# Performance work log

Measured on AMD Instinct MI355X. Metric: run time of the kernel, lower is better.

Reference implementation:

```python
import jax, jax.numpy as jnp
import numpy as np

M_HYP = 20  # RANSAC hypotheses
K_PTS = 4   # points per hypothesis


def _pdsac(pc, apc, idx):
    # pc, apc: [B, 3, N]; idx: [M_HYP*K_PTS] int point indices
    b, _, n = pc.shape
    dt = pc.dtype
    cog = jnp.sum(pc, axis=-1)            # [B,3]  (sum, not mean — faithful)
    c_pc = pc - cog[..., None]
    acog = jnp.sum(apc, axis=-1)
    c_apc = apc - acog[..., None]
    # gather then row-major reshape [B,3,80] -> [B,20,3,4] (mixes channel dim, faithful to torch .view)
    m_pc = c_pc[:, :, idx].reshape(b, M_HYP, 3, K_PTS)
    m_apc = c_apc[:, :, idx].reshape(b, M_HYP, 3, K_PTS)
    cov = jnp.einsum('bmck,bmdk->bmcd', m_pc, m_apc)          # [B,m,3,3]
    u, s, vh = jnp.linalg.svd(cov)
    rot = jnp.matmul(jnp.swapaxes(vh, -1, -2), jnp.swapaxes(u, -1, -2))  # V @ U^T
    rot = jnp.pad(rot, ((0, 0), (0, 0), (0, 1), (0, 0)))      # [B,m,4,3], zero bottom row
    trans = acog - cog                                         # [B,3]
    trans = jnp.broadcast_to(trans[:, None, :], (b, M_HYP, 3))
    trans = jnp.concatenate([trans, jnp.ones((b, M_HYP, 1), dt)], axis=-1)[..., None]  # [B,m,4,1]
    transform = jnp.concatenate([rot, trans], axis=-1)        # [B,m,4,4]
    pc_h = jnp.concatenate([pc, jnp.ones((b, 1, n), dt)], axis=1)   # [B,4,N]
    apc_h = jnp.concatenate([apc, jnp.ones((b, 1, n), dt)], axis=1)
    diff = jnp.einsum('bmcd,bdk->bmck', transform, pc_h) - apc_h[:, None]  # [B,m,4,N]
    errors = jnp.sqrt(jnp.sum(diff * diff, axis=(-2, -1)))    # Frobenius norm, [B,m]
    imin = jnp.argmin(errors, axis=-1)                        # [B]
    best = jnp.take_along_axis(transform, imin[:, None, None, None], axis=1)[:, 0]
    return best                                                # [B,4,4]


def setup_inputs() -> dict:
    key = jax.random.key(0)
    ks = jax.random.split(key, 6)
    bsz, n = 32, 100000
    A = jax.random.normal(ks[0], (bsz, 3, n), dtype=jnp.float32)
    A_g = jax.random.normal(ks[1], (bsz, 3, n), dtype=jnp.float32)
    B = jax.random.normal(ks[2], (bsz, 3, n), dtype=jnp.float32)
    B_g = jax.random.normal(ks[3], (bsz, 3, n), dtype=jnp.float32)
    idx_A = jax.random.randint(ks[4], (M_HYP * K_PTS,), 0, n, dtype=jnp.int32)
    idx_B = jax.random.randint(ks[5], (M_HYP * K_PTS,), 0, n, dtype=jnp.int32)
    return {"A": A, "A_g": A_g, "B": B, "B_g": B_g, "idx_A": idx_A, "idx_B": idx_B}


def reference(A, A_g, B, B_g, idx_A, idx_B):
    T_A = _pdsac(A, A_g, idx_A)
    T_B = _pdsac(B, B_g, idx_B)
    return jnp.matmul(jnp.linalg.inv(T_A), T_B)  # [B,4,4]
```

## Files before the change

### kernel.cpp

```cpp
#include <hip/hip_runtime.h>

#define M_HYP 20
#define AS1 __attribute__((address_space(1)))
#define AS3 __attribute__((address_space(3)))


__device__ __forceinline__ float comb8(const float r[8]) {
    return __fadd_rn(__fadd_rn(__fadd_rn(r[0], r[1]), __fadd_rn(r[2], r[3])),
                     __fadd_rn(__fadd_rn(r[4], r[5]), __fadd_rn(r[6], r[7])));
}

struct RawF { const float* a; };

__device__ __forceinline__ void raw8(const RawF& f, int k, float e[8]) {
    float4 v0 = *(const float4*)(f.a + k);
    float4 v1 = *(const float4*)(f.a + k + 4);
    e[0] = v0.x; e[1] = v0.y; e[2] = v0.z; e[3] = v0.w;
    e[4] = v1.x; e[5] = v1.y; e[6] = v1.z; e[7] = v1.w;
}

__device__ float leaf_raw(const RawF& f, int off, int n) {
    float r[8], e[8];
    raw8(f, off, e);
#pragma unroll
    for (int j = 0; j < 8; ++j) r[j] = e[j];
    for (int i = 8; i < n; i += 8) {
        raw8(f, off + i, e);
#pragma unroll
        for (int j = 0; j < 8; ++j) r[j] = __fadd_rn(r[j], e[j]);
    }
    return comb8(r);
}

__device__ float tree_raw(const RawF& f, int off0, int n0) {
    float lsum[14]; int roff[14], rn[14]; unsigned have = 0;
    int sp = 0, off = off0, n = n0;
    while (true) {
        while (n > 128) {
            int n2 = (n / 2) & ~7;
            roff[sp] = off + n2; rn[sp] = n - n2;
            have &= ~(1u << sp); ++sp;
            n = n2;
        }
        float s = leaf_raw(f, off, n);
        while (sp > 0 && (have & (1u << (sp - 1)))) {
            --sp; s = __fadd_rn(lsum[sp], s);
        }
        if (sp == 0) return s;
        lsum[sp - 1] = s; have |= (1u << (sp - 1));
        off = roff[sp - 1]; n = rn[sp - 1];
    }
}

struct Stg {
    const float *g0, *g1, *g2, *g3, *g4, *g5;
    float (*sm)[264];
    int tile_base;
    int node_end;
    int lane;
    int qs;
    float t0, t1, t2, t3;
};

__device__ __forceinline__ void stage6(Stg& st, int t) {
    int rel = st.lane * 4;
    int src = (rel + 4 <= st.node_end - t) ? (t + rel) : t;
    __builtin_amdgcn_global_load_lds((const AS1 float*)(st.g0 + src), (AS3 float*)&st.sm[0][0], 16, 0, 0);
    __builtin_amdgcn_global_load_lds((const AS1 float*)(st.g1 + src), (AS3 float*)&st.sm[1][0], 16, 0, 0);
    __builtin_amdgcn_global_load_lds((const AS1 float*)(st.g2 + src), (AS3 float*)&st.sm[2][0], 16, 0, 0);
    __builtin_amdgcn_global_load_lds((const AS1 float*)(st.g3 + src), (AS3 float*)&st.sm[3][0], 16, 0, 0);
    __builtin_amdgcn_global_load_lds((const AS1 float*)(st.g4 + src), (AS3 float*)&st.sm[4][0], 16, 0, 0);
    __builtin_amdgcn_global_load_lds((const AS1 float*)(st.g5 + src), (AS3 float*)&st.sm[5][0], 16, 0, 0);
    asm volatile("s_waitcnt vmcnt(0)" ::: "memory");
    __builtin_amdgcn_sched_barrier(0);
}

__device__ __forceinline__ void chunk8(Stg& st, int g, float e[8]) {
    if (g - st.tile_base >= 256) {
        st.tile_base = g;
        stage6(st, g);
    }
    int k = g - st.tile_base;
    float4 a0 = *(const float4*)&st.sm[0][k];
    float4 a1 = *(const float4*)&st.sm[0][k + 4];
    float4 b0 = *(const float4*)&st.sm[1][k];
    float4 b1 = *(const float4*)&st.sm[1][k + 4];
    float4 c0 = *(const float4*)&st.sm[2][k];
    float4 c1 = *(const float4*)&st.sm[2][k + 4];
    const float* qr = &st.sm[st.qs][0];
    float4 d0 = *(const float4*)&qr[k];
    float4 d1 = *(const float4*)&qr[k + 4];
    float px[8] = {a0.x, a0.y, a0.z, a0.w, a1.x, a1.y, a1.z, a1.w};
    float py[8] = {b0.x, b0.y, b0.z, b0.w, b1.x, b1.y, b1.z, b1.w};
    float pz[8] = {c0.x, c0.y, c0.z, c0.w, c1.x, c1.y, c1.z, c1.w};
    float qq[8] = {d0.x, d0.y, d0.z, d0.w, d1.x, d1.y, d1.z, d1.w};
#pragma unroll
    for (int j = 0; j < 8; ++j) {
        float s = __fmul_rn(st.t0, px[j]);
        s = fmaf(st.t1, py[j], s);
        s = fmaf(st.t2, pz[j], s);
        s = __fadd_rn(s, st.t3);
        float d = __fsub_rn(s, qq[j]);
        e[j] = __fmul_rn(d, d);
    }
}

__device__ float leaf_err(Stg& st, int off, int n) {
    float r[8], e[8];
    chunk8(st, off, e);
#pragma unroll
    for (int j = 0; j < 8; ++j) r[j] = e[j];
    for (int i = 8; i < n; i += 8) {
        chunk8(st, off + i, e);
#pragma unroll
        for (int j = 0; j < 8; ++j) r[j] = __fadd_rn(r[j], e[j]);
    }
    return comb8(r);
}

__device__ float tree_err(Stg& st, int off0, int n0) {
    float lsum[14]; int roff[14], rn[14]; unsigned have = 0;
    int sp = 0, off = off0, n = n0;
    while (true) {
        while (n > 128) {
            int n2 = (n / 2) & ~7;
            roff[sp] = off + n2; rn[sp] = n - n2;
            have &= ~(1u << sp); ++sp;
            n = n2;
        }
        float s = leaf_err(st, off, n);
        while (sp > 0 && (have & (1u << (sp - 1)))) {
            --sp; s = __fadd_rn(lsum[sp], s);
        }
        if (sp == 0) return s;
        lsum[sp - 1] = s; have |= (1u << (sp - 1));
        off = roff[sp - 1]; n = rn[sp - 1];
    }
}

#define F32EPS  5.9604645e-8f
#define F32UNFL 1.17549435e-38f

__device__ inline float f32_slapy2(float x, float y) {
    float xa = fabsf(x), ya = fabsf(y);
    float w = fmaxf(xa, ya), z = fminf(xa, ya);
    if (z == 0.0f) return w;
    float t = __fdiv_rn(z, w);
    return __fmul_rn(w, __fsqrt_rn(fmaf(t, t, 1.0f)));
}

__device__ inline float snrm2_2(float x0, float x1) {
    double s = (double)x0 * (double)x0 + (double)x1 * (double)x1;
    return (float)sqrt(s);
}

__device__ inline float f32_slarfg(int nx, float& alpha, float* x) {
    if (nx <= 0) return 0.0f;
    float xnorm = (nx == 1) ? fabsf(x[0]) : snrm2_2(x[0], x[1]);
    if (xnorm == 0.0f) return 0.0f;
    float beta = -copysignf(f32_slapy2(alpha, xnorm), alpha);
    float tau = __fdiv_rn(__fsub_rn(beta, alpha), beta);
    float sc = __fdiv_rn(1.0f, __fsub_rn(alpha, beta));
    for (int i = 0; i < nx; ++i) x[i] = __fmul_rn(x[i], sc);
    alpha = beta;
    return tau;
}

__device__ inline void f32_slartg(float f, float g, float& c, float& s, float& r) {
    float f1 = fabsf(f), g1 = fabsf(g);
    if (g == 0.0f) { c = 1.0f; s = 0.0f; r = f; }
    else if (f == 0.0f) { c = 0.0f; s = copysignf(1.0f, g); r = g1; }
    else {
        float d = __fsqrt_rn(fmaf(f, f, __fmul_rn(g, g)));
        float p = __fdiv_rn(1.0f, d);
        c = __fmul_rn(f1, p);
        s = __fmul_rn(g, copysignf(p, f));
        r = copysignf(d, f);
    }
}

__device__ inline void f32_slas2(float f, float g, float h, float& ssmin, float& ssmax) {
    float fa = fabsf(f), ga = fabsf(g), ha = fabsf(h);
    float fhmn = fminf(fa, ha), fhmx = fmaxf(fa, ha);
    if (fhmn == 0.0f) {
        ssmin = 0.0f;
        if (fhmx == 0.0f) ssmax = ga;
        else {
            float mx = fmaxf(fhmx, ga), mn = fminf(fhmx, ga);
            float t = __fdiv_rn(mn, mx);
            ssmax = __fmul_rn(mx, __fsqrt_rn(fmaf(t, t, 1.0f)));
        }
    } else {
        if (ga < fhmx) {
            float as = __fadd_rn(1.0f, __fdiv_rn(fhmn, fhmx));
            float at = __fdiv_rn(__fsub_rn(fhmx, fhmn), fhmx);
            float q = __fdiv_rn(ga, fhmx);
            float au = __fmul_rn(q, q);
            float c = __fdiv_rn(2.0f, __fadd_rn(__fsqrt_rn(fmaf(as, as, au)),
                                                __fsqrt_rn(fmaf(at, at, au))));
            ssmin = __fmul_rn(fhmn, c);
            ssmax = __fdiv_rn(fhmx, c);
        } else {
            float au = __fdiv_rn(fhmx, ga);
            if (au == 0.0f) {
                ssmin = __fdiv_rn(__fmul_rn(fhmn, fhmx), ga);
                ssmax = ga;
            } else {
                float as = __fadd_rn(1.0f, __fdiv_rn(fhmn, fhmx));
                float at = __fdiv_rn(__fsub_rn(fhmx, fhmn), fhmx);
                float u1 = __fmul_rn(as, au), u2 = __fmul_rn(at, au);
                float c = __fdiv_rn(1.0f, __fadd_rn(__fsqrt_rn(fmaf(u1, u1, 1.0f)),
                                                    __fsqrt_rn(fmaf(u2, u2, 1.0f))));
                ssmin = __fmul_rn(__fmul_rn(fhmn, c), au);
                ssmin = __fadd_rn(ssmin, ssmin);
                ssmax = __fdiv_rn(ga, __fadd_rn(c, c));
            }
        }
    }
}

__device__ inline void f32_slasv2(float f, float g, float h,
                                  float& ssmin, float& ssmax,
                                  float& snr, float& csr, float& snl, float& csl) {
    float ft = f, fa = fabsf(f), ht = h, ha = fabsf(h);
    int pmax = 1;
    bool swp = (ha > fa);
    if (swp) { pmax = 3; float t = ft; ft = ht; ht = t; t = fa; fa = ha; ha = t; }
    float gt = g, ga = fabsf(gt);
    float clt = 0.f, crt = 0.f, slt = 0.f, srt = 0.f;
    if (ga == 0.0f) {
        ssmin = ha; ssmax = fa; clt = 1.0f; crt = 1.0f; slt = 0.0f; srt = 0.0f;
    } else {
        bool gasmal = true;
        if (ga > fa) {
            pmax = 2;
            if (__fdiv_rn(fa, ga) < F32EPS) {
                gasmal = false;
                ssmax = ga;
                if (ha > 1.0f) ssmin = __fdiv_rn(fa, __fdiv_rn(ga, ha));
                else           ssmin = __fmul_rn(__fdiv_rn(fa, ga), ha);
                clt = 1.0f; slt = __fdiv_rn(ht, gt);
                srt = 1.0f; crt = __fdiv_rn(ft, gt);
            }
        }
        if (gasmal) {
            float dd = __fsub_rn(fa, ha);
            float l = (dd == fa) ? 1.0f : __fdiv_rn(dd, fa);
            float vm = __fdiv_rn(gt, ft);
            float t = __fsub_rn(2.0f, l);
            float mm = __fmul_rn(vm, vm);
            float s = __fsqrt_rn(fmaf(t, t, mm));
            float r = (l == 0.0f) ? fabsf(vm) : __fsqrt_rn(fmaf(l, l, mm));
            float a = __fmul_rn(0.5f, __fadd_rn(s, r));
            ssmin = __fdiv_rn(ha, a);
            ssmax = __fmul_rn(fa, a);
            if (mm == 0.0f) {
                if (l == 0.0f) t = __fmul_rn(copysignf(2.0f, ft), copysignf(1.0f, gt));
                else t = __fadd_rn(__fdiv_rn(gt, copysignf(dd, ft)), __fdiv_rn(vm, t));
            } else {
                t = __fmul_rn(__fadd_rn(__fdiv_rn(vm, __fadd_rn(s, t)),
                                        __fdiv_rn(vm, __fadd_rn(r, l))),
                              __fadd_rn(1.0f, a));
            }
            float l2 = __fsqrt_rn(fmaf(t, t, 4.0f));
            crt = __fdiv_rn(2.0f, l2);
            srt = __fdiv_rn(t, l2);
            clt = __fdiv_rn(fmaf(srt, vm, crt), a);
            slt = __fdiv_rn(__fmul_rn(__fdiv_rn(ht, ft), srt), a);
        }
    }
    if (swp) { csl = srt; snl = crt; csr = slt; snr = clt; }
    else     { csl = clt; snl = slt; csr = crt; snr = srt; }
    float tsign = 0.f;
    if (pmax == 1) tsign = __fmul_rn(__fmul_rn(copysignf(1.0f, csr), copysignf(1.0f, csl)), copysignf(1.0f, f));
    if (pmax == 2) tsign = __fmul_rn(__fmul_rn(copysignf(1.0f, snr), copysignf(1.0f, csl)), copysignf(1.0f, g));
    if (pmax == 3) tsign = __fmul_rn(__fmul_rn(copysignf(1.0f, snr), copysignf(1.0f, snl)), copysignf(1.0f, h));
    ssmax = copysignf(ssmax, tsign);
    ssmin = copysignf(ssmin, __fmul_rn(__fmul_rn(tsign, copysignf(1.0f, f)), copysignf(1.0f, h)));
}

__device__ inline void slasr_L(float vt[3][3], int base, int len, const float* c, const float* s, bool fwd) {
    int pairs = len - 1;
    for (int jj = 0; jj < pairs; ++jj) {
        int j = fwd ? jj : (pairs - 1 - jj);
        float cj = c[j], sj = s[j];
        if (cj != 1.0f || sj != 0.0f) {
            for (int i = 0; i < 3; ++i) {
                float temp = vt[base + j + 1][i];
                vt[base + j + 1][i] = fmaf(cj, temp, -__fmul_rn(sj, vt[base + j][i]));
                vt[base + j][i]     = fmaf(sj, temp,  __fmul_rn(cj, vt[base + j][i]));
            }
        }
    }
}
__device__ inline void slasr_R(float u[3][3], int base, int len, const float* c, const float* s, bool fwd) {
    int pairs = len - 1;
    for (int jj = 0; jj < pairs; ++jj) {
        int j = fwd ? jj : (pairs - 1 - jj);
        float cj = c[j], sj = s[j];
        if (cj != 1.0f || sj != 0.0f) {
            for (int i = 0; i < 3; ++i) {
                float temp = u[i][base + j + 1];
                u[i][base + j + 1] = fmaf(cj, temp, -__fmul_rn(sj, u[i][base + j]));
                u[i][base + j]     = fmaf(sj, temp,  __fmul_rn(cj, u[i][base + j]));
            }
        }
    }
}

__device__ void f32_sbdsqr3(float d[3], float e[2], float vt[3][3], float u[3][3]) {
    const int N = 3;
    float TOL = __fmul_rn(10.0f, F32EPS);
    float thresh;
    {
        float sminoa = fabsf(d[0]);
        if (sminoa != 0.0f) {
            float mu = sminoa;
            for (int i = 1; i < N; ++i) {
                mu = __fmul_rn(fabsf(d[i]), __fdiv_rn(mu, __fadd_rn(mu, fabsf(e[i - 1]))));
                sminoa = fminf(sminoa, mu);
                if (sminoa == 0.0f) break;
            }
        }
        sminoa = __fdiv_rn(sminoa, __fsqrt_rn((float)N));
        thresh = fmaxf(__fmul_rn(TOL, sminoa), __fmul_rn(54.0f, F32UNFL));
    }
    int m = N, oldll = -1, oldm = -1, idir = 0;
    int guard = 0;
    while (true) {
        if (m <= 1) break;
        if (++guard > 400) break;
        int ll = 0;
        float smax_blk = fabsf(d[m - 1]);
        bool split = false;
        for (int lll = 1; lll <= m - 1; ++lll) {
            ll = m - lll;
            float abss = fabsf(d[ll - 1]);
            float abse = fabsf(e[ll - 1]);
            if (abse <= thresh) { split = true; break; }
            smax_blk = fmaxf(smax_blk, fmaxf(abss, abse));
        }
        if (split) {
            e[ll - 1] = 0.0f;
            if (ll == m - 1) { m -= 1; continue; }
            ll += 1;
        } else ll = 1;
        if (ll == m - 1) {
            float sigmn, sigmx, sinr, cosr, sinl, cosl;
            f32_slasv2(d[m - 2], e[m - 2], d[m - 1], sigmn, sigmx, sinr, cosr, sinl, cosl);
            d[m - 2] = sigmx; e[m - 2] = 0.0f; d[m - 1] = sigmn;
            for (int i = 0; i < 3; ++i) {
                float x = vt[m - 2][i], y = vt[m - 1][i];
                float temp = fmaf(cosr, x, __fmul_rn(sinr, y));
                vt[m - 1][i] = fmaf(cosr, y, -__fmul_rn(sinr, x));
                vt[m - 2][i] = temp;
            }
            for (int i = 0; i < 3; ++i) {
                float x = u[i][m - 2], y = u[i][m - 1];
                float temp = fmaf(cosl, x, __fmul_rn(sinl, y));
                u[i][m - 1] = fmaf(cosl, y, -__fmul_rn(sinl, x));
                u[i][m - 2] = temp;
            }
            m -= 2;
            continue;
        }
        if (ll > oldm || m < oldll)
            idir = (fabsf(d[ll - 1]) >= fabsf(d[m - 1])) ? 1 : 2;
        float sminl = 0.0f;
        bool deflated = false;
        if (idir == 1) {
            if (fabsf(e[m - 2]) <= __fmul_rn(fabsf(TOL), fabsf(d[m - 1]))) { e[m - 2] = 0.0f; continue; }
            float mu = fabsf(d[ll - 1]);
            sminl = mu;
            for (int lll = ll; lll <= m - 1; ++lll) {
                if (fabsf(e[lll - 1]) <= __fmul_rn(TOL, mu)) { e[lll - 1] = 0.0f; deflated = true; break; }
                mu = __fmul_rn(fabsf(d[lll]), __fdiv_rn(mu, __fadd_rn(mu, fabsf(e[lll - 1]))));
                sminl = fminf(sminl, mu);
            }
        } else {
            if (fabsf(e[ll - 1]) <= __fmul_rn(fabsf(TOL), fabsf(d[ll - 1]))) { e[ll - 1] = 0.0f; continue; }
            float mu = fabsf(d[m - 1]);
            sminl = mu;
            for (int lll = m - 1; lll >= ll; --lll) {
                if (fabsf(e[lll - 1]) <= __fmul_rn(TOL, mu)) { e[lll - 1] = 0.0f; deflated = true; break; }
                mu = __fmul_rn(fabsf(d[lll - 1]), __fdiv_rn(mu, __fadd_rn(mu, fabsf(e[lll - 1]))));
                sminl = fminf(sminl, mu);
            }
        }
        if (deflated) continue;
        oldll = ll; oldm = m;
        float shift = 0.0f, rdum;
        {
            float lhs = __fmul_rn(__fmul_rn((float)N, TOL), __fdiv_rn(sminl, smax_blk));
            float rhs = fmaxf(F32EPS, __fmul_rn(0.01f, TOL));
            if (lhs <= rhs) shift = 0.0f;
            else {
                float sll;
                if (idir == 1) { sll = fabsf(d[ll - 1]); f32_slas2(d[m - 2], e[m - 2], d[m - 1], shift, rdum); }
                else           { sll = fabsf(d[m - 1]);  f32_slas2(d[ll - 1], e[ll - 1], d[ll], shift, rdum); }
                if (sll > 0.0f) {
                    float q = __fdiv_rn(shift, sll);
                    if (__fmul_rn(q, q) < F32EPS) shift = 0.0f;
                }
            }
        }
        float wcs[2], wsn[2], wocs[2], wosn[2];
        int len = m - ll + 1;
        if (shift == 0.0f) {
            if (idir == 1) {
                float cs = 1.0f, oldcs = 1.0f, sn, oldsn = 0.0f, r;
                for (int i = ll; i <= m - 1; ++i) {
                    float fin = __fmul_rn(d[i - 1], cs);
                    f32_slartg(fin, e[i - 1], cs, sn, r);
                    if (i > ll) e[i - 2] = __fmul_rn(oldsn, r);
                    float g = __fmul_rn(d[i], sn);
                    f32_slartg(__fmul_rn(oldcs, r), g, oldcs, oldsn, d[i - 1]);
                    wcs[i - ll] = cs; wsn[i - ll] = sn; wocs[i - ll] = oldcs; wosn[i - ll] = oldsn;
                }
                float h = __fmul_rn(d[m - 1], cs);
                d[m - 1] = __fmul_rn(h, oldcs);
                e[m - 2] = __fmul_rn(h, oldsn);
                slasr_L(vt, ll - 1, len, wcs, wsn, true);
                slasr_R(u, ll - 1, len, wocs, wosn, true);
                if (fabsf(e[m - 2]) <= thresh) e[m - 2] = 0.0f;
            } else {
                float cs = 1.0f, oldcs = 1.0f, sn, oldsn = 0.0f, r;
                for (int i = m; i >= ll + 1; --i) {
                    float fin = __fmul_rn(d[i - 1], cs);
                    f32_slartg(fin, e[i - 2], cs, sn, r);
                    if (i < m) e[i - 1] = __fmul_rn(oldsn, r);
                    float g = __fmul_rn(d[i - 2], sn);
                    f32_slartg(__fmul_rn(oldcs, r), g, oldcs, oldsn, d[i - 1]);
                    wcs[i - ll - 1] = cs; wsn[i - ll - 1] = -sn;
                    wocs[i - ll - 1] = oldcs; wosn[i - ll - 1] = -oldsn;
                }
                float h = __fmul_rn(d[ll - 1], cs);
                d[ll - 1] = __fmul_rn(h, oldcs);
                e[ll - 1] = __fmul_rn(h, oldsn);
                slasr_L(vt, ll - 1, len, wocs, wosn, false);
                slasr_R(u, ll - 1, len, wcs, wsn, false);
                if (fabsf(e[ll - 1]) <= thresh) e[ll - 1] = 0.0f;
            }
        } else {
            if (idir == 1) {
                float f = __fmul_rn(__fsub_rn(fabsf(d[ll - 1]), shift),
                                    __fadd_rn(copysignf(1.0f, d[ll - 1]), __fdiv_rn(shift, d[ll - 1])));
                float g = e[ll - 1];
                float cosr, sinr, cosl, sinl, r;
                for (int i = ll; i <= m - 1; ++i) {
                    f32_slartg(f, g, cosr, sinr, r);
                    if (i > ll) e[i - 2] = r;
                    f        = fmaf(cosr, d[i - 1],  __fmul_rn(sinr, e[i - 1]));
                    e[i - 1] = fmaf(cosr, e[i - 1], -__fmul_rn(sinr, d[i - 1]));
                    g = __fmul_rn(sinr, d[i]);
                    d[i] = __fmul_rn(cosr, d[i]);
                    f32_slartg(f, g, cosl, sinl, r);
                    d[i - 1] = r;
                    f    = fmaf(cosl, e[i - 1],  __fmul_rn(sinl, d[i]));
                    d[i] = fmaf(cosl, d[i],     -__fmul_rn(sinl, e[i - 1]));
                    if (i < m - 1) {
                        g = __fmul_rn(sinl, e[i]);
                        e[i] = __fmul_rn(cosl, e[i]);
                    }
                    wcs[i - ll] = cosr; wsn[i - ll] = sinr; wocs[i - ll] = cosl; wosn[i - ll] = sinl;
                }
                e[m - 2] = f;
                if (fabsf(e[m - 2]) <= thresh) e[m - 2] = 0.0f;
                slasr_L(vt, ll - 1, len, wcs, wsn, true);
                slasr_R(u, ll - 1, len, wocs, wosn, true);
            } else {
                float f = __fmul_rn(__fsub_rn(fabsf(d[m - 1]), shift),
                                    __fadd_rn(copysignf(1.0f, d[m - 1]), __fdiv_rn(shift, d[m - 1])));
                float g = e[m - 2];
                float cosr, sinr, cosl, sinl, r;
                for (int i = m; i >= ll + 1; --i) {
                    f32_slartg(f, g, cosr, sinr, r);
                    if (i < m) e[i - 1] = r;
                    f        = fmaf(cosr, d[i - 1],  __fmul_rn(sinr, e[i - 2]));
                    e[i - 2] = fmaf(cosr, e[i - 2], -__fmul_rn(sinr, d[i - 1]));
                    g = __fmul_rn(sinr, d[i - 2]);
                    d[i - 2] = __fmul_rn(cosr, d[i - 2]);
                    f32_slartg(f, g, cosl, sinl, r);
                    d[i - 1] = r;
                    f        = fmaf(cosl, e[i - 2],  __fmul_rn(sinl, d[i - 2]));
                    d[i - 2] = fmaf(cosl, d[i - 2], -__fmul_rn(sinl, e[i - 2]));
                    if (i > ll + 1) {
                        g = __fmul_rn(sinl, e[i - 3]);
                        e[i - 3] = __fmul_rn(cosl, e[i - 3]);
                    }
                    wcs[i - ll - 1] = cosr; wsn[i - ll - 1] = -sinr;
                    wocs[i - ll - 1] = cosl; wosn[i - ll - 1] = -sinl;
                }
                e[ll - 1] = f;
                if (fabsf(e[ll - 1]) <= thresh) e[ll - 1] = 0.0f;
                slasr_L(vt, ll - 1, len, wocs, wosn, false);
                slasr_R(u, ll - 1, len, wcs, wsn, false);
            }
        }
    }
    for (int i = 0; i < N; ++i) {
        if (d[i] < 0.0f) {
            d[i] = -d[i];
            for (int j = 0; j < 3; ++j) vt[i][j] = __fmul_rn(-1.0f, vt[i][j]);
        }
    }
    for (int i = 1; i <= N - 1; ++i) {
        int isub = 0; float smin = d[0];
        for (int j = 1; j <= N - i; ++j)
            if (d[j] <= smin) { isub = j; smin = d[j]; }
        int tgt = N - i;
        if (isub != tgt) {
            d[isub] = d[tgt]; d[tgt] = smin;
            for (int j = 0; j < 3; ++j) { float t = vt[isub][j]; vt[isub][j] = vt[tgt][j]; vt[tgt][j] = t; }
            for (int j = 0; j < 3; ++j) { float t = u[j][isub]; u[j][isub] = u[j][tgt]; u[j][tgt] = t; }
        }
    }
}

__device__ void sgesdd3_rot(float a[3][3], float rot[3][3]) {
    float d[3], e[2], tauq2, tauq1, taup1;
    {
        float x[2] = { a[1][0], a[2][0] };
        float alpha = a[0][0];
        tauq1 = f32_slarfg(2, alpha, x);
        a[1][0] = x[0]; a[2][0] = x[1];
        d[0] = alpha;
        if (tauq1 != 0.0f) {
            float v1 = a[1][0], v2 = a[2][0];
            for (int j = 1; j < 3; ++j) {
                float w = a[0][j];
                w = fmaf(a[1][j], v1, w);
                w = fmaf(a[2][j], v2, w);
                float tmp = __fmul_rn(-tauq1, w);
                a[0][j] = __fadd_rn(a[0][j], tmp);
                a[1][j] = fmaf(v1, tmp, a[1][j]);
                a[2][j] = fmaf(v2, tmp, a[2][j]);
            }
        }
    }
    {
        float x[1] = { a[0][2] };
        float alpha = a[0][1];
        taup1 = f32_slarfg(1, alpha, x);
        a[0][2] = x[0];
        e[0] = alpha; a[0][1] = alpha;
        if (taup1 != 0.0f) {
            float v1 = a[0][2];
            float w1 = fmaf(a[1][2], v1, a[1][1]);
            float w2 = fmaf(a[2][2], v1, a[2][1]);
            float nt = -taup1;
            float t0 = __fmul_rn(nt, 1.0f);
            a[1][1] = fmaf(w1, t0, a[1][1]);
            a[2][1] = fmaf(w2, t0, a[2][1]);
            float t1 = __fmul_rn(nt, v1);
            a[1][2] = fmaf(w1, t1, a[1][2]);
            a[2][2] = fmaf(w2, t1, a[2][2]);
        }
    }
    {
        float x[1] = { a[2][1] };
        float alpha = a[1][1];
        tauq2 = f32_slarfg(1, alpha, x);
        a[2][1] = x[0];
        d[1] = alpha;
        if (tauq2 != 0.0f) {
            float v1 = a[2][1];
            float w = a[1][2];
            w = fmaf(a[2][2], v1, w);
            float tmp = __fmul_rn(-tauq2, w);
            a[1][2] = __fadd_rn(a[1][2], tmp);
            a[2][2] = fmaf(v1, tmp, a[2][2]);
        }
        e[1] = a[1][2];
    }
    d[2] = a[2][2];
    float u[3][3], vt[3][3];
    for (int i = 0; i < 3; ++i)
        for (int j = 0; j < 3; ++j) { u[i][j] = (i == j) ? 1.0f : 0.0f; vt[i][j] = (i == j) ? 1.0f : 0.0f; }
    f32_sbdsqr3(d, e, vt, u);
    if (tauq2 != 0.0f) {
        float v1 = a[2][1];
        for (int j = 0; j < 3; ++j) {
            float w = u[1][j];
            w = fmaf(u[2][j], v1, w);
            float tmp = __fmul_rn(-tauq2, w);
            u[1][j] = __fadd_rn(u[1][j], tmp);
            u[2][j] = fmaf(v1, tmp, u[2][j]);
        }
    }
    if (tauq1 != 0.0f) {
        float v1 = a[1][0], v2 = a[2][0];
        for (int j = 0; j < 3; ++j) {
            float w = u[0][j];
            w = fmaf(u[1][j], v1, w);
            w = fmaf(u[2][j], v2, w);
            float tmp = __fmul_rn(-tauq1, w);
            u[0][j] = __fadd_rn(u[0][j], tmp);
            u[1][j] = fmaf(v1, tmp, u[1][j]);
            u[2][j] = fmaf(v2, tmp, u[2][j]);
        }
    }
    if (taup1 != 0.0f) {
        float v1 = a[0][2];
        float w0 = fmaf(vt[0][2], v1, vt[0][1]);
        float w1 = fmaf(vt[1][2], v1, vt[1][1]);
        float w2 = fmaf(vt[2][2], v1, vt[2][1]);
        float nt = -taup1;
        float t0 = __fmul_rn(nt, 1.0f);
        vt[0][1] = fmaf(w0, t0, vt[0][1]);
        vt[1][1] = fmaf(w1, t0, vt[1][1]);
        vt[2][1] = fmaf(w2, t0, vt[2][1]);
        float t1 = __fmul_rn(nt, v1);
        vt[0][2] = fmaf(w0, t1, vt[0][2]);
        vt[1][2] = fmaf(w1, t1, vt[1][2]);
        vt[2][2] = fmaf(w2, t1, vt[2][2]);
    }
    for (int i = 0; i < 3; ++i)
        for (int j = 0; j < 3; ++j) {
            float acc = __fmul_rn(vt[0][i], u[j][0]);
            acc = __fadd_rn(acc, __fmul_rn(vt[1][i], u[j][1]));
            acc = __fadd_rn(acc, __fmul_rn(vt[2][i], u[j][2]));
            rot[i][j] = acc;
        }
}


__global__ __launch_bounds__(384)
void cog_kernel(const float* __restrict__ A, const float* __restrict__ Ag,
                const float* __restrict__ Bc, const float* __restrict__ Bg,
                int Bn, long long N, float* __restrict__ cogs )
{
    int inst = blockIdx.x >> 2;
    int qt = blockIdx.x & 3;
    int pair = inst / Bn, b = inst % Bn;
    const float* P = (pair ? Bc : A)  + (long long)b * 3 * N;
    const float* Q = (pair ? Bg : Ag) + (long long)b * 3 * N;
    int ch = threadIdx.x >> 6, lane = threadIdx.x & 63;
    RawF f;
    f.a = (ch < 3) ? (P + (long long)ch * N) : (Q + (long long)(ch - 3) * N);
    int node = qt * 64 + lane;
    int off = 0, n = (int)N;
#pragma unroll
    for (int lvl = 7; lvl >= 0; --lvl) {
        int n2 = (n / 2) & ~7;
        if ((node >> lvl) & 1) { off += n2; n -= n2; } else n = n2;
    }
    float s = tree_raw(f, off, n);
#pragma unroll
    for (int lvl = 0; lvl < 6; ++lvl)
        s = __fadd_rn(s, __shfl_down(s, 1 << lvl, 64));
    if (lane == 0) cogs[(inst * 6 + ch) * 4 + qt] = s;
}

__global__ __launch_bounds__(64)
void hypoT_kernel(const float* __restrict__ A, const float* __restrict__ Ag,
                  const float* __restrict__ Bc, const float* __restrict__ Bg,
                  const int* __restrict__ idxA, const int* __restrict__ idxB,
                  const float* __restrict__ cogs, int Bn, long long N,
                  float* __restrict__ Tall)
{
    int inst = blockIdx.x;
    int pair = inst / Bn, b = inst % Bn;
    const float* P = (pair ? Bc : A)  + (long long)b * 3 * N;
    const float* Q = (pair ? Bg : Ag) + (long long)b * 3 * N;
    const int* idx = pair ? idxB : idxA;

    int m = threadIdx.x;
    if (m >= M_HYP) return;

    float S[6];
#pragma unroll
    for (int ch = 0; ch < 6; ++ch) {
        const float* g = cogs + (inst * 6 + ch) * 4;
        S[ch] = __fadd_rn(__fadd_rn(g[0], g[1]), __fadd_rn(g[2], g[3]));
    }

    float x[12], y[12];
#pragma unroll
    for (int j = 0; j < 12; ++j) {
        int f = m * 12 + j, c = f / 80, i = f % 80;
        int id = idx[i];
        x[j] = __fsub_rn(P[(long long)c * N + id], S[c]);
        y[j] = __fsub_rn(Q[(long long)c * N + id], S[3 + c]);
    }
    float cov[3][3];
#pragma unroll
    for (int r = 0; r < 3; ++r)
#pragma unroll
        for (int dcol = 0; dcol < 3; ++dcol) {
            float s = __fmul_rn(x[r * 4 + 0], y[dcol * 4 + 0]);
            s = __fadd_rn(s, __fmul_rn(x[r * 4 + 1], y[dcol * 4 + 1]));
            s = __fadd_rn(s, __fmul_rn(x[r * 4 + 2], y[dcol * 4 + 2]));
            s = __fadd_rn(s, __fmul_rn(x[r * 4 + 3], y[dcol * 4 + 3]));
            cov[r][dcol] = s;
        }

    float rot[3][3];
    sgesdd3_rot(cov, rot);

    float* T = Tall + ((long long)inst * M_HYP + m) * 12;
#pragma unroll
    for (int r = 0; r < 3; ++r) {
        T[r * 4 + 0] = rot[r][0];
        T[r * 4 + 1] = rot[r][1];
        T[r * 4 + 2] = rot[r][2];
        T[r * 4 + 3] = __fsub_rn(S[3 + r], S[r]);
    }
}

__global__ __launch_bounds__(64)
void err_partial(const float* __restrict__ A, const float* __restrict__ Ag,
                 const float* __restrict__ Bc, const float* __restrict__ Bg,
                 const float* __restrict__ Tall, int Bn, long long N,
                 float* __restrict__ partials )
{
    int inst = blockIdx.x >> 6;
    int node = blockIdx.x & 63;
    int pair = inst / Bn, b = inst % Bn;
    const float* P = (pair ? Bc : A)  + (long long)b * 3 * N;
    const float* Q = (pair ? Bg : Ag) + (long long)b * 3 * N;

    int lane = threadIdx.x;
    int combo = lane < 60 ? lane : 59;
    int m = combo / 3, c = combo - m * 3;
    const float* T = Tall + ((long long)inst * M_HYP + m) * 12;

    __shared__ float sm[6][264];

    int off = 0, n = (int)N;
#pragma unroll
    for (int lvl = 5; lvl >= 0; --lvl) {
        int n2 = (n / 2) & ~7;
        if ((node >> lvl) & 1) { off += n2; n -= n2; } else n = n2;
    }

    Stg st;
    st.g0 = P; st.g1 = P + N; st.g2 = P + 2 * N;
    st.g3 = Q; st.g4 = Q + N; st.g5 = Q + 2 * N;
    st.sm = sm;
    st.node_end = off + n;
    st.lane = lane;
    st.qs = 3 + c;
    st.t0 = T[c * 4 + 0]; st.t1 = T[c * 4 + 1];
    st.t2 = T[c * 4 + 2]; st.t3 = T[c * 4 + 3];
    st.tile_base = off;
    stage6(st, off);

    float s = tree_err(st, off, n);
    if (lane < 60)
        partials[(((long long)inst * M_HYP + m) * 3 + c) * 64 + node] = s;
}

__global__ __launch_bounds__(64)
void final_kernel(const float* __restrict__ partials, const float* __restrict__ Tall,
                  int Bn, float* __restrict__ out)
{
    int b = blockIdx.x;
    __shared__ float errsh[2][M_HYP];
    int t = threadIdx.x;
    if (t < 2 * M_HYP) {
        int pair = t / M_HYP, m = t % M_HYP;
        int inst = pair * Bn + b;
        float S[3];
#pragma unroll
        for (int c = 0; c < 3; ++c) {
            const float* g = partials + (((long long)inst * M_HYP + m) * 3 + c) * 64;
            float v[64];
#pragma unroll
            for (int i = 0; i < 64; ++i) v[i] = g[i];
#pragma unroll
            for (int lvl = 0; lvl < 6; ++lvl) {
#pragma unroll
                for (int i = 0; i < 32; ++i)
                    if (i < (32 >> lvl)) v[i] = __fadd_rn(v[2 * i], v[2 * i + 1]);
            }
            S[c] = v[0];
        }
        errsh[pair][m] = __fsqrt_rn(__fadd_rn(__fadd_rn(S[0], S[1]), S[2]));
    }
    __syncthreads();
    if (t == 0) {
        int bm[2];
#pragma unroll
        for (int pair = 0; pair < 2; ++pair) {
            int bi = 0; float be = errsh[pair][0];
            for (int mm = 1; mm < M_HYP; ++mm)
                if (errsh[pair][mm] < be) { be = errsh[pair][mm]; bi = mm; }
            bm[pair] = bi;
        }
        float TA[16], TB[16];
        const float* TsA = Tall + ((long long)(0 * Bn + b) * M_HYP + bm[0]) * 12;
        const float* TsB = Tall + ((long long)(1 * Bn + b) * M_HYP + bm[1]) * 12;
        for (int j = 0; j < 12; ++j) { TA[j] = TsA[j]; TB[j] = TsB[j]; }
        TA[12] = TA[13] = TA[14] = 0.0f; TA[15] = 1.0f;
        TB[12] = TB[13] = TB[14] = 0.0f; TB[15] = 1.0f;

        double M[4][8];
        for (int i = 0; i < 4; ++i) {
            for (int j = 0; j < 4; ++j) { M[i][j] = (double)TA[i * 4 + j]; M[i][4 + j] = 0.0; }
            M[i][4 + i] = 1.0;
        }
        for (int cc = 0; cc < 4; ++cc) {
            int piv = cc; double mx = fabs(M[cc][cc]);
            for (int r = cc + 1; r < 4; ++r) { double v = fabs(M[r][cc]); if (v > mx) { mx = v; piv = r; } }
            if (piv != cc)
                for (int j = 0; j < 8; ++j) { double tt = M[cc][j]; M[cc][j] = M[piv][j]; M[piv][j] = tt; }
            double dd = 1.0 / M[cc][cc];
            for (int j = 0; j < 8; ++j) M[cc][j] *= dd;
            for (int r = 0; r < 4; ++r) {
                if (r == cc) continue;
                double ff = M[r][cc];
                for (int j = 0; j < 8; ++j) M[r][j] -= ff * M[cc][j];
            }
        }
        for (int i = 0; i < 4; ++i)
            for (int j = 0; j < 4; ++j) {
                double s = 0.0;
                for (int k = 0; k < 4; ++k) s += M[i][4 + k] * (double)TB[k * 4 + j];
                out[b * 16 + i * 4 + j] = (float)s;
            }
    }
}

extern "C" void kernel_launch(void* const* d_in, const int* in_sizes, int n_in,
                              void* d_out, int out_size, void* d_ws, size_t ws_size,
                              hipStream_t stream) {
    const float* A    = (const float*)d_in[0];
    const float* Ag   = (const float*)d_in[1];
    const float* Bc   = (const float*)d_in[2];
    const float* Bg   = (const float*)d_in[3];
    const int*   idxA = (const int*)d_in[4];
    const int*   idxB = (const int*)d_in[5];
    float* out = (float*)d_out;

    int Bn = out_size / 16;
    long long N = (long long)in_sizes[0] / (3LL * Bn);
    int inst = 2 * Bn;

    float* cogs     = (float*)d_ws;
    float* Tall     = cogs + (size_t)inst * 6 * 4;
    float* partials = Tall + (size_t)inst * M_HYP * 12;

    cog_kernel  <<<inst * 4,  384, 0, stream>>>(A, Ag, Bc, Bg, Bn, N, cogs);
    hypoT_kernel<<<inst,       64, 0, stream>>>(A, Ag, Bc, Bg, idxA, idxB, cogs, Bn, N, Tall);
    err_partial <<<inst * 64,  64, 0, stream>>>(A, Ag, Bc, Bg, Tall, Bn, N, partials);
    final_kernel<<<Bn,         64, 0, stream>>>(partials, Tall, Bn, out);
}
```

Before: 149.0 us.

## Double-buffer LDS tile staging to prefetch next tile during compute

```diff
diff --git a/kernel.cpp b/kernel.cpp
--- a/kernel.cpp
+++ b/kernel.cpp
@@ -54,40 +54,50 @@
 
 struct Stg {
     const float *g0, *g1, *g2, *g3, *g4, *g5;
-    float (*sm)[264];
+    float (*sm0)[264];
+    float (*sm1)[264];
     int tile_base;
     int node_end;
+    int cur;
     int lane;
     int qs;
     float t0, t1, t2, t3;
 };
 
-__device__ __forceinline__ void stage6(Stg& st, int t) {
+__device__ __forceinline__ void issue6(Stg& st, int bufi, int t) {
     int rel = st.lane * 4;
     int src = (rel + 4 <= st.node_end - t) ? (t + rel) : t;
-    __builtin_amdgcn_global_load_lds((const AS1 float*)(st.g0 + src), (AS3 float*)&st.sm[0][0], 16, 0, 0);
-    __builtin_amdgcn_global_load_lds((const AS1 float*)(st.g1 + src), (AS3 float*)&st.sm[1][0], 16, 0, 0);
-    __builtin_amdgcn_global_load_lds((const AS1 float*)(st.g2 + src), (AS3 float*)&st.sm[2][0], 16, 0, 0);
-    __builtin_amdgcn_global_load_lds((const AS1 float*)(st.g3 + src), (AS3 float*)&st.sm[3][0], 16, 0, 0);
-    __builtin_amdgcn_global_load_lds((const AS1 float*)(st.g4 + src), (AS3 float*)&st.sm[4][0], 16, 0, 0);
-    __builtin_amdgcn_global_load_lds((const AS1 float*)(st.g5 + src), (AS3 float*)&st.sm[5][0], 16, 0, 0);
-    asm volatile("s_waitcnt vmcnt(0)" ::: "memory");
-    __builtin_amdgcn_sched_barrier(0);
+    float (*dst)[264] = bufi ? st.sm1 : st.sm0;
+    __builtin_amdgcn_global_load_lds((const AS1 float*)(st.g0 + src), (AS3 float*)&dst[0][0], 16, 0, 0);
+    __builtin_amdgcn_global_load_lds((const AS1 float*)(st.g1 + src), (AS3 float*)&dst[1][0], 16, 0, 0);
+    __builtin_amdgcn_global_load_lds((const AS1 float*)(st.g2 + src), (AS3 float*)&dst[2][0], 16, 0, 0);
+    __builtin_amdgcn_global_load_lds((const AS1 float*)(st.g3 + src), (AS3 float*)&dst[3][0], 16, 0, 0);
+    __builtin_amdgcn_global_load_lds((const AS1 float*)(st.g4 + src), (AS3 float*)&dst[4][0], 16, 0, 0);
+    __builtin_amdgcn_global_load_lds((const AS1 float*)(st.g5 + src), (AS3 float*)&dst[5][0], 16, 0, 0);
 }
 
 __device__ __forceinline__ void chunk8(Stg& st, int g, float e[8]) {
     if (g - st.tile_base >= 256) {
         st.tile_base = g;
-        stage6(st, g);
-    }
+        st.cur ^= 1;
+        int nxt = g + 256;
+        if (nxt < st.node_end) {
+            issue6(st, st.cur ^ 1, nxt);
+            asm volatile("s_waitcnt vmcnt(6)" ::: "memory");
+        } else {
+            asm volatile("s_waitcnt vmcnt(0)" ::: "memory");
+        }
+        __builtin_amdgcn_sched_barrier(0);
+    }
+    float (*smc)[264] = st.cur ? st.sm1 : st.sm0;
     int k = g - st.tile_base;
-    float4 a0 = *(const float4*)&st.sm[0][k];
-    float4 a1 = *(const float4*)&st.sm[0][k + 4];
-    float4 b0 = *(const float4*)&st.sm[1][k];
-    float4 b1 = *(const float4*)&st.sm[1][k + 4];
-    float4 c0 = *(const float4*)&st.sm[2][k];
-    float4 c1 = *(const float4*)&st.sm[2][k + 4];
-    const float* qr = &st.sm[st.qs][0];
+    float4 a0 = *(const float4*)&smc[0][k];
+    float4 a1 = *(const float4*)&smc[0][k + 4];
+    float4 b0 = *(const float4*)&smc[1][k];
+    float4 b1 = *(const float4*)&smc[1][k + 4];
+    float4 c0 = *(const float4*)&smc[2][k];
+    float4 c1 = *(const float4*)&smc[2][k + 4];
+    const float* qr = &smc[st.qs][0];
     float4 d0 = *(const float4*)&qr[k];
     float4 d1 = *(const float4*)&qr[k + 4];
     float px[8] = {a0.x, a0.y, a0.z, a0.w, a1.x, a1.y, a1.z, a1.w};
@@ -725,7 +735,8 @@
     int m = combo / 3, c = combo - m * 3;
     const float* T = Tall + ((long long)inst * M_HYP + m) * 12;
 
-    __shared__ float sm[6][264];
+    __shared__ float smA[6][264];
+    __shared__ float smB[6][264];
 
     int off = 0, n = (int)N;
 #pragma unroll
@@ -737,14 +748,23 @@
     Stg st;
     st.g0 = P; st.g1 = P + N; st.g2 = P + 2 * N;
     st.g3 = Q; st.g4 = Q + N; st.g5 = Q + 2 * N;
-    st.sm = sm;
+    st.sm0 = smA; st.sm1 = smB;
     st.node_end = off + n;
     st.lane = lane;
     st.qs = 3 + c;
     st.t0 = T[c * 4 + 0]; st.t1 = T[c * 4 + 1];
     st.t2 = T[c * 4 + 2]; st.t3 = T[c * 4 + 3];
     st.tile_base = off;
-    stage6(st, off);
+    st.cur = 0;
+
+    issue6(st, 0, off);
+    if (off + 256 < st.node_end) {
+        issue6(st, 1, off + 256);
+        asm volatile("s_waitcnt vmcnt(6)" ::: "memory");
+    } else {
+        asm volatile("s_waitcnt vmcnt(0)" ::: "memory");
+    }
+    __builtin_amdgcn_sched_barrier(0);
 
     float s = tree_err(st, off, n);
     if (lane < 60)
```

Result: slower. 164.6 us (+10.4%).
